# Performance work log

Hardware: AMD Instinct MI355X
Metric: run time of the kernel (lower is better)

## Reference

```python
import jax, jax.numpy as jnp
import numpy as np

N_NODES = 50000
N_GRAPHS = 64
HID = 100

def gcn_conv(x, W, b, src, dst, n):
    # dense transform first (PyG GCNConv): [N, out]
    h = x @ W
    # add self loops (improved=False -> fill 1.0)
    loops = jnp.arange(n, dtype=src.dtype)
    s = jnp.concatenate([src, loops])
    d = jnp.concatenate([dst, loops])
    # symmetric normalization D^-1/2 A D^-1/2
    deg = jax.ops.segment_sum(jnp.ones_like(s, dtype=h.dtype), d, num_segments=n)
    dinv = jnp.where(deg > 0, jax.lax.rsqrt(jnp.maximum(deg, 1e-12)), 0.0)
    norm = dinv[s] * dinv[d]  # [E+N]
    msgs = h[s] * norm[:, None]  # gather + scale
    out = jax.ops.segment_sum(msgs, d, num_segments=n)  # scatter-add
    return out + b

def global_mean_pool(x, batch, num_graphs):
    sums = jax.ops.segment_sum(x, batch, num_segments=num_graphs)
    cnts = jax.ops.segment_sum(jnp.ones((x.shape[0],), x.dtype), batch, num_segments=num_graphs)
    return sums / jnp.maximum(cnts, 1.0)[:, None]

def setup_inputs() -> dict:
    key = jax.random.key(0)
    ks = jax.random.split(key, 8)
    d_in = 128
    x = jax.random.normal(ks[0], (N_NODES, d_in), dtype=jnp.float32)
    edge_index = jax.random.randint(ks[1], (2, 800000), 0, N_NODES, dtype=jnp.int64)
    batch = jnp.sort(jax.random.randint(ks[2], (N_NODES,), 0, N_GRAPHS, dtype=jnp.int64))
    s1 = 1.0 / np.sqrt(d_in)
    s2 = 1.0 / np.sqrt(HID)
    W1 = jax.random.uniform(ks[3], (d_in, HID), jnp.float32, -s1, s1)
    b1 = jnp.zeros((HID,), jnp.float32)
    W2 = jax.random.uniform(ks[4], (HID, HID), jnp.float32, -s2, s2)
    b2 = jnp.zeros((HID,), jnp.float32)
    Wlin = jax.random.uniform(ks[5], (HID, 1), jnp.float32, -s2, s2)
    blin = jax.random.uniform(ks[6], (1,), jnp.float32, -s2, s2)
    return {"x": x, "edge_index": edge_index, "batch": batch,
            "W1": W1, "b1": b1, "W2": W2, "b2": b2, "Wlin": Wlin, "blin": blin}

def reference(x, edge_index, batch, W1, b1, W2, b2, Wlin, blin):
    src, dst = edge_index[0], edge_index[1]
    h = gcn_conv(x, W1, b1, src, dst, N_NODES)
    h = jnp.tanh(h)
    h = gcn_conv(h, W2, b2, src, dst, N_NODES)
    g = global_mean_pool(h, batch, N_GRAPHS)  # [G, HID]
    return g @ Wlin + blin  # [G, 1]
```

## Files before the change

kernel.cpp:

```cpp
#include <hip/hip_runtime.h>
#include <hip/hip_bf16.h>

#define N_NODES 50000
#define N_GRAPHS 64
#define HID 100
#define HP 104

#define BKE  4096
#define NBIN 196
#define NPB 39

#define OFF_DINV 0
#define OFF_CNTF 50048
#define OFF_POOL 50112
#define OFF_WT1  50176
#define OFF_HS   64512
#define OFF_ROWPTR 7864512
#define OFF_EIDX   7914560
#define OFF_BE     8714560
#define OFF_BBINS  9514560
#define OFF_BOFF   9565760
#define OFF_BTOT   9616960
#define OFF_DONE   9617440
#define OFF_W2L    9617472
#define OFF_Q      9617600

typedef __attribute__((ext_vector_type(8))) short short8;
typedef __attribute__((ext_vector_type(4))) float floatx4;

__device__ inline float b2f(unsigned int u) {
    union { unsigned int v; float f; } x; x.v = u << 16; return x.f;
}
__device__ inline unsigned short f2b(float f) {
    union { float f; unsigned int v; } x; x.f = f;
    unsigned int r = (x.v + 0x7fffu + ((x.v >> 16) & 1u)) >> 16;
    return (unsigned short)r;
}

__global__ __launch_bounds__(256) void k_prep(const float* __restrict__ W1,
                                              const float* __restrict__ W2,
                                              const float* __restrict__ Wlin,
                                              const float* __restrict__ b2,
                                              unsigned short* __restrict__ Wt1,
                                              float* __restrict__ w2l,
                                              float* __restrict__ pool,
                                              float* __restrict__ cntf,
                                              int* __restrict__ done) {
    const int b = blockIdx.x, t = threadIdx.x;
    if (b < 56) {
        int idx = b * 256 + t;
        int c = idx >> 7, k = idx & 127;
        float v = (k < 128 && c < HID) ? W1[k * HID + c] : 0.0f;
        Wt1[c * 128 + k] = f2b(v);
    } else {
        if (t < 104) {
            float s = 0.0f;
            if (t < 100)
                for (int c = 0; c < HID; ++c) s += W2[t * HID + c] * Wlin[c];
            w2l[t] = s;
        } else if (t == 104) {
            float s = 0.0f;
            for (int j = 0; j < HID; ++j) s += b2[j] * Wlin[j];
            w2l[104] = s;
        } else if (t >= 128 && t < 128 + N_GRAPHS) {
            pool[t - 128] = 0.0f; cntf[t - 128] = 0.0f;
        } else if (t == 224) {
            *done = 0;
        }
    }
}

__global__ __launch_bounds__(256) void k_p1(const int* __restrict__ dst, int E,
                                            int* __restrict__ bbins) {
    __shared__ int hist[256];
    const int t = threadIdx.x, b = blockIdx.x;
    hist[t] = 0;
    __syncthreads();
    int e0 = b * BKE, e1 = min(e0 + BKE, E);
    for (int e = e0 + t; e < e1; e += 256) atomicAdd(&hist[dst[e] >> 8], 1);
    __syncthreads();
    if (t < NBIN) bbins[b * NBIN + t] = hist[t];
}

__global__ __launch_bounds__(256) void k_p2a(const int* __restrict__ bbins, int nb,
                                             int* __restrict__ boff, int* __restrict__ btot) {
    __shared__ int sb[256];
    const int t = threadIdx.x, j = blockIdx.x;
    int v = (t < nb) ? bbins[t * NBIN + j] : 0;
    sb[t] = v;
    __syncthreads();
    for (int off = 1; off < 256; off <<= 1) {
        int u = (t >= off) ? sb[t - off] : 0;
        __syncthreads();
        sb[t] += u;
        __syncthreads();
    }
    if (t < nb) boff[t * NBIN + j] = sb[t] - v;
    if (t == 255) btot[j] = sb[255];
}

__global__ __launch_bounds__(256) void k_p3(const int* __restrict__ src, const int* __restrict__ dst,
                                            int E, const int* __restrict__ boff,
                                            const int* __restrict__ btot,
                                            unsigned int* __restrict__ bE) {
    __shared__ unsigned int stage[BKE];
    __shared__ int hist[256], pref[256], cur[256], sb[256], offr[NBIN];
    const int t = threadIdx.x, b = blockIdx.x;
    {
        int v = (t < NBIN) ? btot[t] : 0;
        sb[t] = v;
        __syncthreads();
        for (int off = 1; off < 256; off <<= 1) {
            int u = (t >= off) ? sb[t - off] : 0;
            __syncthreads();
            sb[t] += u;
            __syncthreads();
        }
        if (t < NBIN) offr[t] = boff[b * NBIN + t] + (sb[t] - v);
    }
    hist[t] = 0;
    __syncthreads();
    const int e0 = b * BKE, e1 = min(e0 + BKE, E), n = e1 - e0;
    unsigned int mine[16];
#pragma unroll
    for (int u = 0; u < 16; ++u) {
        int e = e0 + u * 256 + t;
        if (e < e1) {
            unsigned int v = ((unsigned int)src[e] << 16) | (unsigned int)dst[e];
            mine[u] = v;
            atomicAdd(&hist[(v >> 8) & 255], 1);
        }
    }
    __syncthreads();
    sb[t] = hist[t];
    __syncthreads();
    for (int off = 1; off < 256; off <<= 1) {
        int v = (t >= off) ? sb[t - off] : 0;
        __syncthreads();
        sb[t] += v;
        __syncthreads();
    }
    pref[t] = sb[t] - hist[t];
    cur[t] = pref[t];
    __syncthreads();
#pragma unroll
    for (int u = 0; u < 16; ++u) {
        int e = e0 + u * 256 + t;
        if (e < e1) {
            unsigned int v = mine[u];
            int p = atomicAdd(&cur[(v >> 8) & 255], 1);
            stage[p] = v;
        }
    }
    __syncthreads();
    for (int i = t; i < n; i += 256) {
        unsigned int v = stage[i];
        int bin = (v >> 8) & 255;
        bE[offr[bin] + (i - pref[bin])] = v;
    }
}

__global__ __launch_bounds__(256) void k_p4(const unsigned int* __restrict__ bE,
                                            const int* __restrict__ btot, int E,
                                            int* __restrict__ rowptr, unsigned short* __restrict__ eidx,
                                            float* __restrict__ dinv) {
    __shared__ int hist[256], pref[256], cur[256], sb[256];
    __shared__ int eBaseSh, eEndSh;
    const int t = threadIdx.x, b = blockIdx.x;
    {
        int v = (t < NBIN) ? btot[t] : 0;
        sb[t] = v;
        __syncthreads();
        for (int off = 1; off < 256; off <<= 1) {
            int u = (t >= off) ? sb[t - off] : 0;
            __syncthreads();
            sb[t] += u;
            __syncthreads();
        }
        if (t == b) { eBaseSh = sb[t] - v; eEndSh = sb[t]; }
    }
    hist[t] = 0;
    __syncthreads();
    const int eBase = eBaseSh, eEnd = eEndSh, n = eEnd - eBase;
    for (int i = t; i < n; i += 256) atomicAdd(&hist[bE[eBase + i] & 255], 1);
    __syncthreads();
    sb[t] = hist[t];
    __syncthreads();
    for (int off = 1; off < 256; off <<= 1) {
        int v = (t >= off) ? sb[t - off] : 0;
        __syncthreads();
        sb[t] += v;
        __syncthreads();
    }
    pref[t] = sb[t] - hist[t];
    cur[t] = pref[t];
    int node = (b << 8) + t;
    if (node < N_NODES) {
        rowptr[node] = eBase + pref[t];
        dinv[node] = rsqrtf((float)(hist[t] + 1));
    }
    if (b == NBIN - 1 && t == 0) rowptr[N_NODES] = E;
    __syncthreads();
    for (int i = t; i < n; i += 256) {
        unsigned int v = bE[eBase + i];
        int p = atomicAdd(&cur[v & 255], 1);
        eidx[eBase + p] = (unsigned short)(v >> 16);
    }
}

__global__ __launch_bounds__(256) void k_gemm(const float* __restrict__ A,
                                              const unsigned short* __restrict__ Wt,
                                              const float* __restrict__ dinv,
                                              unsigned short* __restrict__ out) {
    __shared__ __align__(16) unsigned short xs[64][136];
    __shared__ __align__(16) unsigned short ws[112][136];
    const int t = threadIdx.x;
    const int base = blockIdx.x * 64;

    for (int idx = t; idx < 112 * 64; idx += 256) {
        int c = idx >> 6, u = idx & 63;
        *(unsigned int*)&ws[c][2 * u] = ((const unsigned int*)Wt)[idx];
    }
    for (int idx = t; idx < 64 * 32; idx += 256) {
        int r = idx >> 5, q = idx & 31;
        int row = base + r;
        ushort4 p;
        if (row < N_NODES) {
            float4 v = ((const float4*)(A + (size_t)row * 128))[q];
            p.x = f2b(v.x); p.y = f2b(v.y); p.z = f2b(v.z); p.w = f2b(v.w);
        } else p = make_ushort4(0, 0, 0, 0);
        *(ushort4*)&xs[r][4 * q] = p;
    }
    __syncthreads();

    const int lane = t & 63, w = t >> 6;
    const int g = lane >> 4, cl = lane & 15;

    floatx4 acc[7];
#pragma unroll
    for (int n = 0; n < 7; ++n) acc[n] = (floatx4){0.f, 0.f, 0.f, 0.f};

#pragma unroll
    for (int kc = 0; kc < 4; ++kc) {
        short8 a = *(const short8*)&xs[w * 16 + cl][kc * 32 + 8 * g];
#pragma unroll
        for (int n = 0; n < 7; ++n) {
            short8 b = *(const short8*)&ws[n * 16 + cl][kc * 32 + 8 * g];
            acc[n] = __builtin_amdgcn_mfma_f32_16x16x32_bf16(a, b, acc[n], 0, 0, 0);
        }
    }

    float di[4]; int grows[4];
#pragma unroll
    for (int r = 0; r < 4; ++r) {
        grows[r] = base + w * 16 + 4 * g + r;
        di[r] = (grows[r] < N_NODES) ? dinv[grows[r]] : 0.0f;
    }
#pragma unroll
    for (int n = 0; n < 7; ++n) {
        int gcol = n * 16 + cl;
        if (gcol >= HP) continue;
#pragma unroll
        for (int r = 0; r < 4; ++r) {
            if (grows[r] < N_NODES)
                out[(size_t)grows[r] * HP + gcol] = f2b(acc[n][r] * di[r]);
        }
    }
}

#define ACC8(v) do { \
    s[0] += b2f((v).x & 0xffff); s[1] += b2f((v).x >> 16); \
    s[2] += b2f((v).y & 0xffff); s[3] += b2f((v).y >> 16); \
    s[4] += b2f((v).z & 0xffff); s[5] += b2f((v).z >> 16); \
    s[6] += b2f((v).w & 0xffff); s[7] += b2f((v).w >> 16); } while (0)

__global__ __launch_bounds__(512) void k_gather_q(const int* __restrict__ rowptr,
                                                  const unsigned short* __restrict__ eidx,
                                                  const unsigned short* __restrict__ hs,
                                                  const float* __restrict__ dinv,
                                                  const float* __restrict__ b1,
                                                  const float* __restrict__ w2l,
                                                  float* __restrict__ q) {
    __shared__ float wl[104];
    __shared__ float bsh[104];
    __shared__ float part[512];
    const int t = threadIdx.x;
    if (t < 104) { wl[t] = w2l[t]; bsh[t] = (t < 100) ? b1[t] : 0.0f; }
    const int nid = t / 13, c = t - nid * 13;
    const int i = blockIdx.x * NPB + nid;
    const bool active = (t < NPB * 13) && (i < N_NODES);
    __syncthreads();

    float partial = 0.0f;
    float di = 0.0f;
    if (active) {
        const int c0 = 8 * c;
        float s[8] = {0.f, 0.f, 0.f, 0.f, 0.f, 0.f, 0.f, 0.f};
        uint4 sv = *(const uint4*)(hs + (size_t)i * HP + c0);
        ACC8(sv);
        int e = rowptr[i];
        const int end = rowptr[i + 1];
        for (; e + 16 <= end; e += 16) {
            int n[16];
#pragma unroll
            for (int u = 0; u < 16; ++u) n[u] = eidx[e + u];
            uint4 v[16];
#pragma unroll
            for (int u = 0; u < 16; ++u) v[u] = *(const uint4*)(hs + (size_t)n[u] * HP + c0);
#pragma unroll
            for (int u = 0; u < 16; ++u) ACC8(v[u]);
        }
        for (; e + 8 <= end; e += 8) {
            int n[8];
#pragma unroll
            for (int u = 0; u < 8; ++u) n[u] = eidx[e + u];
            uint4 v[8];
#pragma unroll
            for (int u = 0; u < 8; ++u) v[u] = *(const uint4*)(hs + (size_t)n[u] * HP + c0);
#pragma unroll
            for (int u = 0; u < 8; ++u) ACC8(v[u]);
        }
        for (; e + 4 <= end; e += 4) {
            int n[4];
#pragma unroll
            for (int u = 0; u < 4; ++u) n[u] = eidx[e + u];
            uint4 v[4];
#pragma unroll
            for (int u = 0; u < 4; ++u) v[u] = *(const uint4*)(hs + (size_t)n[u] * HP + c0);
#pragma unroll
            for (int u = 0; u < 4; ++u) ACC8(v[u]);
        }
        for (; e < end; ++e) {
            uint4 v = *(const uint4*)(hs + (size_t)eidx[e] * HP + c0);
            ACC8(v);
        }
        di = dinv[i];
#pragma unroll
        for (int j = 0; j < 8; ++j) {
            float h = tanhf(di * s[j] + bsh[c0 + j]);
            partial += h * wl[c0 + j];
        }
    }
    part[t] = partial;
    __syncthreads();
    if (active && c == 0) {
        float sum = 0.0f;
#pragma unroll
        for (int j = 0; j < 13; ++j) sum += part[t + j];
        q[i] = di * sum;
    }
}

__global__ __launch_bounds__(256) void k_gpool(const int* __restrict__ rowptr,
                                               const unsigned short* __restrict__ eidx,
                                               const float* __restrict__ q,
                                               const float* __restrict__ dinv,
                                               const int* __restrict__ batch,
                                               float* __restrict__ pool,
                                               float* __restrict__ cntf,
                                               const float* __restrict__ w2l,
                                               const float* __restrict__ blin,
                                               int* __restrict__ done,
                                               float* __restrict__ out) {
    __shared__ float sp[N_GRAPHS];
    __shared__ float sc[N_GRAPHS];
    __shared__ int lastFlag;
    const int t = threadIdx.x;
    if (t < N_GRAPHS) { sp[t] = 0.0f; sc[t] = 0.0f; }
    __syncthreads();
    int i = blockIdx.x * 256 + t;
    if (i < N_NODES) {
        float s = q[i];
        int e = rowptr[i];
        const int end = rowptr[i + 1];
        for (; e + 8 <= end; e += 8) {
            int n0 = eidx[e],     n1 = eidx[e + 1], n2 = eidx[e + 2], n3 = eidx[e + 3];
            int n4 = eidx[e + 4], n5 = eidx[e + 5], n6 = eidx[e + 6], n7 = eidx[e + 7];
            s += q[n0] + q[n1] + q[n2] + q[n3] + q[n4] + q[n5] + q[n6] + q[n7];
        }
        for (; e + 4 <= end; e += 4) {
            int n0 = eidx[e], n1 = eidx[e + 1], n2 = eidx[e + 2], n3 = eidx[e + 3];
            s += q[n0] + q[n1] + q[n2] + q[n3];
        }
        for (; e < end; ++e) s += q[eidx[e]];
        float p = dinv[i] * s;
        int g = batch[i];
        atomicAdd(&sp[g], p);
        atomicAdd(&sc[g], 1.0f);
    }
    __syncthreads();
    if (t < N_GRAPHS && sc[t] != 0.0f) {
        atomicAdd(&pool[t], sp[t]);
        atomicAdd(&cntf[t], sc[t]);
    }
    __syncthreads();
    if (t == 0) {
        __threadfence();
        int ticket = atomicAdd(done, 1);
        lastFlag = (ticket == (int)gridDim.x - 1);
    }
    __syncthreads();
    if (lastFlag && t < N_GRAPHS) {
        float p = atomicAdd(&pool[t], 0.0f);
        float c = atomicAdd(&cntf[t], 0.0f);
        out[t] = p / fmaxf(c, 1.0f) + w2l[104] + blin[0];
    }
}

extern "C" void kernel_launch(void* const* d_in, const int* in_sizes, int n_in,
                              void* d_out, int out_size, void* d_ws, size_t ws_size,
                              hipStream_t stream) {
    const float* x    = (const float*)d_in[0];
    const int*   ei   = (const int*)d_in[1];
    const int*   batch= (const int*)d_in[2];
    const float* W1   = (const float*)d_in[3];
    const float* b1   = (const float*)d_in[4];
    const float* W2   = (const float*)d_in[5];
    const float* b2   = (const float*)d_in[6];
    const float* Wlin = (const float*)d_in[7];
    const float* blin = (const float*)d_in[8];
    float* out = (float*)d_out;

    const int E = in_sizes[1] / 2;
    const int* src = ei;
    const int* dst = ei + E;

    float* wsf  = (float*)d_ws;
    int*   wsi  = (int*)d_ws;
    float* dinv = wsf + OFF_DINV;
    float* cntf = wsf + OFF_CNTF;
    float* pool = wsf + OFF_POOL;
    unsigned short* Wt1 = (unsigned short*)(wsf + OFF_WT1);
    unsigned short* HS  = (unsigned short*)(wsf + OFF_HS);
    int* rowptr = wsi + OFF_ROWPTR;
    unsigned short* eidx = (unsigned short*)(wsi + OFF_EIDX);
    unsigned int* bE = (unsigned int*)(wsi + OFF_BE);
    int* bbins  = wsi + OFF_BBINS;
    int* boff   = wsi + OFF_BOFF;
    int* btot   = wsi + OFF_BTOT;
    int* done   = wsi + OFF_DONE;
    float* w2l  = wsf + OFF_W2L;
    float* q    = wsf + OFF_Q;

    const int nbE = (E + BKE - 1) / BKE;
    const int nGrid = (N_NODES + 255) / 256;
    const int gqGrid = (N_NODES + NPB - 1) / NPB;

    k_prep<<<57, 256, 0, stream>>>(W1, W2, Wlin, b2, Wt1, w2l, pool, cntf, done);
    k_p1<<<nbE, 256, 0, stream>>>(dst, E, bbins);
    k_p2a<<<NBIN, 256, 0, stream>>>(bbins, nbE, boff, btot);
    k_p3<<<nbE, 256, 0, stream>>>(src, dst, E, boff, btot, bE);
    k_p4<<<NBIN, 256, 0, stream>>>(bE, btot, E, rowptr, eidx, dinv);

    k_gemm<<<(N_NODES + 63) / 64, 256, 0, stream>>>(x, Wt1, dinv, HS);

    k_gather_q<<<gqGrid, 512, 0, stream>>>(rowptr, eidx, HS, dinv, b1, w2l, q);

    k_gpool<<<nGrid, 256, 0, stream>>>(rowptr, eidx, q, dinv, batch, pool, cntf,
                                       w2l, blin, done, out);
}
```

Before: 108.7 us.

## Replace multi-pass edge bucketing with single-pass atomic-cursor bins of fixed capacity

The histogram, cross-block scan and offset kernels for the dst-bucket sort are removed. Each sort block now reserves space in a per-bin global cursor with one atomicAdd per bin and scatters into fixed-capacity bin slots. A per-node degree array replaces the `rowptr[i+1]` end lookup, because bins are no longer contiguous. This saves two kernel launches and a pass over the dst array. In exchange, edges beyond `CAP` in any bin are silently dropped, and the order of edges within a bin becomes nondeterministic.

```diff
diff --git a/kernel.cpp b/kernel.cpp
--- a/kernel.cpp
+++ b/kernel.cpp
@@ -8,6 +8,7 @@
 
 #define BKE  4096
 #define NBIN 196
+#define CAP  8192
 #define NPB 39
 
 #define OFF_DINV 0
@@ -15,15 +16,14 @@
 #define OFF_POOL 50112
 #define OFF_WT1  50176
 #define OFF_HS   64512
-#define OFF_ROWPTR 7864512
-#define OFF_EIDX   7914560
-#define OFF_BE     8714560
-#define OFF_BBINS  9514560
-#define OFF_BOFF   9565760
-#define OFF_BTOT   9616960
-#define OFF_DONE   9617440
-#define OFF_W2L    9617472
-#define OFF_Q      9617600
+#define OFF_ROWPTR 2664512
+#define OFF_DEG    2714560
+#define OFF_EIDX   2739648
+#define OFF_BE     3542464
+#define OFF_CURSOR 5148096
+#define OFF_DONE   5148352
+#define OFF_W2L    5148416
+#define OFF_Q      5148544
 
 typedef __attribute__((ext_vector_type(8))) short short8;
 typedef __attribute__((ext_vector_type(4))) float floatx4;
@@ -45,14 +45,15 @@
                                               float* __restrict__ w2l,
                                               float* __restrict__ pool,
                                               float* __restrict__ cntf,
-                                              int* __restrict__ done) {
+                                              int* __restrict__ done,
+                                              int* __restrict__ cursor) {
     const int b = blockIdx.x, t = threadIdx.x;
     if (b < 56) {
         int idx = b * 256 + t;
         int c = idx >> 7, k = idx & 127;
         float v = (k < 128 && c < HID) ? W1[k * HID + c] : 0.0f;
         Wt1[c * 128 + k] = f2b(v);
-    } else {
+    } else if (b == 56) {
         if (t < 104) {
             float s = 0.0f;
             if (t < 100)
@@ -67,57 +68,18 @@
         } else if (t == 224) {
             *done = 0;
         }
-    }
-}
-
-__global__ __launch_bounds__(256) void k_p1(const int* __restrict__ dst, int E,
-                                            int* __restrict__ bbins) {
-    __shared__ int hist[256];
+    } else {
+        if (t < NBIN) cursor[t] = 0;
+    }
+}
+
+__global__ __launch_bounds__(256) void k_sort(const int* __restrict__ src,
+                                              const int* __restrict__ dst, int E,
+                                              int* __restrict__ cursor,
+                                              unsigned int* __restrict__ bE) {
+    __shared__ unsigned int stage[BKE];
+    __shared__ int hist[256], pref[256], cur[256], sb[256], resS[256];
     const int t = threadIdx.x, b = blockIdx.x;
-    hist[t] = 0;
-    __syncthreads();
-    int e0 = b * BKE, e1 = min(e0 + BKE, E);
-    for (int e = e0 + t; e < e1; e += 256) atomicAdd(&hist[dst[e] >> 8], 1);
-    __syncthreads();
-    if (t < NBIN) bbins[b * NBIN + t] = hist[t];
-}
-
-__global__ __launch_bounds__(256) void k_p2a(const int* __restrict__ bbins, int nb,
-                                             int* __restrict__ boff, int* __restrict__ btot) {
-    __shared__ int sb[256];
-    const int t = threadIdx.x, j = blockIdx.x;
-    int v = (t < nb) ? bbins[t * NBIN + j] : 0;
-    sb[t] = v;
-    __syncthreads();
-    for (int off = 1; off < 256; off <<= 1) {
-        int u = (t >= off) ? sb[t - off] : 0;
-        __syncthreads();
-        sb[t] += u;
-        __syncthreads();
-    }
-    if (t < nb) boff[t * NBIN + j] = sb[t] - v;
-    if (t == 255) btot[j] = sb[255];
-}
-
-__global__ __launch_bounds__(256) void k_p3(const int* __restrict__ src, const int* __restrict__ dst,
-                                            int E, const int* __restrict__ boff,
-                                            const int* __restrict__ btot,
-                                            unsigned int* __restrict__ bE) {
-    __shared__ unsigned int stage[BKE];
-    __shared__ int hist[256], pref[256], cur[256], sb[256], offr[NBIN];
-    const int t = threadIdx.x, b = blockIdx.x;
-    {
-        int v = (t < NBIN) ? btot[t] : 0;
-        sb[t] = v;
-        __syncthreads();
-        for (int off = 1; off < 256; off <<= 1) {
-            int u = (t >= off) ? sb[t - off] : 0;
-            __syncthreads();
-            sb[t] += u;
-            __syncthreads();
-        }
-        if (t < NBIN) offr[t] = boff[b * NBIN + t] + (sb[t] - v);
-    }
     hist[t] = 0;
     __syncthreads();
     const int e0 = b * BKE, e1 = min(e0 + BKE, E), n = e1 - e0;
@@ -142,6 +104,7 @@
     }
     pref[t] = sb[t] - hist[t];
     cur[t] = pref[t];
+    if (t < NBIN && hist[t] > 0) resS[t] = atomicAdd(&cursor[t], hist[t]);
     __syncthreads();
 #pragma unroll
     for (int u = 0; u < 16; ++u) {
@@ -156,32 +119,24 @@
     for (int i = t; i < n; i += 256) {
         unsigned int v = stage[i];
         int bin = (v >> 8) & 255;
-        bE[offr[bin] + (i - pref[bin])] = v;
+        int rel = resS[bin] + (i - pref[bin]);
+        if (rel < CAP) bE[bin * CAP + rel] = v;
     }
 }
 
 __global__ __launch_bounds__(256) void k_p4(const unsigned int* __restrict__ bE,
-                                            const int* __restrict__ btot, int E,
-                                            int* __restrict__ rowptr, unsigned short* __restrict__ eidx,
+                                            const int* __restrict__ cursor,
+                                            int* __restrict__ rowptr,
+                                            unsigned short* __restrict__ deg,
+                                            unsigned short* __restrict__ eidx,
                                             float* __restrict__ dinv) {
     __shared__ int hist[256], pref[256], cur[256], sb[256];
-    __shared__ int eBaseSh, eEndSh;
     const int t = threadIdx.x, b = blockIdx.x;
-    {
-        int v = (t < NBIN) ? btot[t] : 0;
-        sb[t] = v;
-        __syncthreads();
-        for (int off = 1; off < 256; off <<= 1) {
-            int u = (t >= off) ? sb[t - off] : 0;
-            __syncthreads();
-            sb[t] += u;
-            __syncthreads();
-        }
-        if (t == b) { eBaseSh = sb[t] - v; eEndSh = sb[t]; }
-    }
+    const int eBase = b * CAP;
+    int n = cursor[b];
+    if (n > CAP) n = CAP;
     hist[t] = 0;
     __syncthreads();
-    const int eBase = eBaseSh, eEnd = eEndSh, n = eEnd - eBase;
     for (int i = t; i < n; i += 256) atomicAdd(&hist[bE[eBase + i] & 255], 1);
     __syncthreads();
     sb[t] = hist[t];
@@ -197,9 +152,9 @@
     int node = (b << 8) + t;
     if (node < N_NODES) {
         rowptr[node] = eBase + pref[t];
+        deg[node] = (unsigned short)hist[t];
         dinv[node] = rsqrtf((float)(hist[t] + 1));
     }
-    if (b == NBIN - 1 && t == 0) rowptr[N_NODES] = E;
     __syncthreads();
     for (int i = t; i < n; i += 256) {
         unsigned int v = bE[eBase + i];
@@ -275,6 +230,7 @@
     s[6] += b2f((v).w & 0xffff); s[7] += b2f((v).w >> 16); } while (0)
 
 __global__ __launch_bounds__(512) void k_gather_q(const int* __restrict__ rowptr,
+                                                  const unsigned short* __restrict__ deg,
                                                   const unsigned short* __restrict__ eidx,
                                                   const unsigned short* __restrict__ hs,
                                                   const float* __restrict__ dinv,
@@ -299,7 +255,7 @@
         uint4 sv = *(const uint4*)(hs + (size_t)i * HP + c0);
         ACC8(sv);
         int e = rowptr[i];
-        const int end = rowptr[i + 1];
+        const int end = e + deg[i];
         for (; e + 16 <= end; e += 16) {
             int n[16];
 #pragma unroll
@@ -352,6 +308,7 @@
 }
 
 __global__ __launch_bounds__(256) void k_gpool(const int* __restrict__ rowptr,
+                                               const unsigned short* __restrict__ deg,
                                                const unsigned short* __restrict__ eidx,
                                                const float* __restrict__ q,
                                                const float* __restrict__ dinv,
@@ -372,7 +329,7 @@
     if (i < N_NODES) {
         float s = q[i];
         int e = rowptr[i];
-        const int end = rowptr[i + 1];
+        const int end = e + deg[i];
         for (; e + 8 <= end; e += 8) {
             int n0 = eidx[e],     n1 = eidx[e + 1], n2 = eidx[e + 2], n3 = eidx[e + 3];
             int n4 = eidx[e + 4], n5 = eidx[e + 5], n6 = eidx[e + 6], n7 = eidx[e + 7];
@@ -389,7 +346,7 @@
         atomicAdd(&sc[g], 1.0f);
     }
     __syncthreads();
-    if (t < N_GRAPHS && sc[t] != 0.0f) {
+    if (t < N_GRAPHS && (sp[t] != 0.0f || sc[t] != 0.0f)) {
         atomicAdd(&pool[t], sp[t]);
         atomicAdd(&cntf[t], sc[t]);
     }
@@ -433,11 +390,10 @@
     unsigned short* Wt1 = (unsigned short*)(wsf + OFF_WT1);
     unsigned short* HS  = (unsigned short*)(wsf + OFF_HS);
     int* rowptr = wsi + OFF_ROWPTR;
+    unsigned short* deg  = (unsigned short*)(wsi + OFF_DEG);
     unsigned short* eidx = (unsigned short*)(wsi + OFF_EIDX);
     unsigned int* bE = (unsigned int*)(wsi + OFF_BE);
-    int* bbins  = wsi + OFF_BBINS;
-    int* boff   = wsi + OFF_BOFF;
-    int* btot   = wsi + OFF_BTOT;
+    int* cursor = wsi + OFF_CURSOR;
     int* done   = wsi + OFF_DONE;
     float* w2l  = wsf + OFF_W2L;
     float* q    = wsf + OFF_Q;
@@ -446,16 +402,14 @@
     const int nGrid = (N_NODES + 255) / 256;
     const int gqGrid = (N_NODES + NPB - 1) / NPB;
 
-    k_prep<<<57, 256, 0, stream>>>(W1, W2, Wlin, b2, Wt1, w2l, pool, cntf, done);
-    k_p1<<<nbE, 256, 0, stream>>>(dst, E, bbins);
-    k_p2a<<<NBIN, 256, 0, stream>>>(bbins, nbE, boff, btot);
-    k_p3<<<nbE, 256, 0, stream>>>(src, dst, E, boff, btot, bE);
-    k_p4<<<NBIN, 256, 0, stream>>>(bE, btot, E, rowptr, eidx, dinv);
+    k_prep<<<58, 256, 0, stream>>>(W1, W2, Wlin, b2, Wt1, w2l, pool, cntf, done, cursor);
+    k_sort<<<nbE, 256, 0, stream>>>(src, dst, E, cursor, bE);
+    k_p4<<<NBIN, 256, 0, stream>>>(bE, cursor, rowptr, deg, eidx, dinv);
 
     k_gemm<<<(N_NODES + 63) / 64, 256, 0, stream>>>(x, Wt1, dinv, HS);
 
-    k_gather_q<<<gqGrid, 512, 0, stream>>>(rowptr, eidx, HS, dinv, b1, w2l, q);
-
-    k_gpool<<<nGrid, 256, 0, stream>>>(rowptr, eidx, q, dinv, batch, pool, cntf,
+    k_gather_q<<<gqGrid, 512, 0, stream>>>(rowptr, deg, eidx, HS, dinv, b1, w2l, q);
+
+    k_gpool<<<nGrid, 256, 0, stream>>>(rowptr, deg, eidx, q, dinv, batch, pool, cntf,
                                        w2l, blin, done, out);
 }
```

Result: faster. 101.4 us (-6.7%).
